# Performance work log

Measured on AMD Instinct MI355X. Metric: run time of the kernel, lower is better.

## Reference

```python
import jax, jax.numpy as jnp
from jax import lax
import numpy as np

B, L, H, V = 256, 2048, 128, 32000
THR = 0.4      # energy_threshold
LN_EPS = 1e-5  # torch LayerNorm default


def setup_inputs() -> dict:
    key = jax.random.key(0)
    ks = jax.random.split(key, 12)
    s = lambda k, shp, scale: (jax.random.normal(k, shp, dtype=jnp.float32) * scale)
    return {
        "seq": jax.random.randint(ks[0], (B, L), 0, V),
        "embed": s(ks[1], (V, H), 0.02),
        "W1": s(ks[2], (H, 2 * H), H ** -0.5),
        "b1": jnp.zeros((2 * H,), jnp.float32),
        "W2": s(ks[3], (2 * H, H), (2 * H) ** -0.5),
        "b2": jnp.zeros((H,), jnp.float32),
        "gamma": jnp.ones((H,), jnp.float32),
        "beta": jnp.zeros((H,), jnp.float32),
        "Wrp": s(ks[4], (H, H), H ** -0.5),
        "brp": jnp.zeros((H,), jnp.float32),
        "Wout": s(ks[5], (H, V), H ** -0.5),
        "bout": jnp.zeros((V,), jnp.float32),
    }


def _encode(seq, embed, W1, b1, W2, b2, gamma, beta):
    e = embed[seq]                                         # [B,L,H]
    ff = jnp.maximum(e @ W1 + b1, 0.0) @ W2 + b2           # [B,L,H]
    y = e + ff
    mu = y.mean(-1, keepdims=True)
    var = ((y - mu) ** 2).mean(-1, keepdims=True)
    return (y - mu) * lax.rsqrt(var + LN_EPS) * gamma + beta


def reference(seq, embed, W1, b1, W2, b2, gamma, beta, Wrp, brp, Wout, bout):
    h_all = _encode(seq, embed, W1, b1, W2, b2, gamma, beta)  # [B,L,H]

    def step(M, k):
        # k = v = h_all[:, t, :]  -> [B,H]
        v = k
        vp = jnp.einsum('bij,bj->bi', M, k)
        error = v - vp / (jnp.sum(k * k, axis=-1, keepdims=True) + 1e-6)
        gate = (jnp.linalg.norm(error, axis=-1)
                > THR * jnp.linalg.norm(v, axis=-1)).astype(M.dtype)  # [B]
        M = M + gate[:, None, None] * jnp.einsum('bi,bj->bij', error, k)
        return M, None

    M0 = jnp.zeros((B, H, H), h_all.dtype)
    ks = jnp.swapaxes(h_all[:, :-1, :], 0, 1)               # [L-1,B,H]
    M_fin, _ = lax.scan(step, M0, ks)
    r = jnp.einsum('bij,bj->bi', M_fin, h_all[:, -1, :])    # [B,H]
    return (r @ Wrp + brp) @ Wout + bout                    # [B,V]
```

## Files before the change

kernel.cpp:

```cpp
#include <hip/hip_runtime.h>
#include <hip/hip_bf16.h>


#define BB 256
#define LL 2048
#define HH 128
#define VV 32000
#define RS 136

typedef float f32x2 __attribute__((ext_vector_type(2)));

__device__ __forceinline__ void dma16(const float* g, float* l) {
  __builtin_amdgcn_global_load_lds(
      (const __attribute__((address_space(1))) void*)g,
      (__attribute__((address_space(3))) void*)l,
      16, 0, 0);
}

template <int CTRL>
__device__ __forceinline__ float dppadd(float x) {
  int y = __builtin_amdgcn_update_dpp(0, __float_as_int(x), CTRL, 0xF, 0xF, true);
  return x + __int_as_float(y);
}

__device__ __forceinline__ void pkfma(f32x2& d, f32x2 a, f32x2 b) {
  asm("v_pk_fma_f32 %0, %1, %2, %0" : "+v"(d) : "v"(a), "v"(b));
}

__device__ __forceinline__ void barrier_lgkm() {
  asm volatile("s_waitcnt lgkmcnt(0)\n\ts_barrier" ::: "memory");
}
__device__ __forceinline__ void wait_vmN(int n) {
  if (n == 5)      asm volatile("s_waitcnt vmcnt(5)" ::: "memory");
  else if (n == 4) asm volatile("s_waitcnt vmcnt(4)" ::: "memory");
  else if (n == 3) asm volatile("s_waitcnt vmcnt(3)" ::: "memory");
  else if (n == 2) asm volatile("s_waitcnt vmcnt(2)" ::: "memory");
  else if (n == 1) asm volatile("s_waitcnt vmcnt(1)" ::: "memory");
  else             asm volatile("s_waitcnt vmcnt(0)" ::: "memory");
}

__global__ __launch_bounds__(256, 1) void build_htab_kernel(
    const float* __restrict__ embed,
    const float* __restrict__ W1,
    const float* __restrict__ b1,
    const float* __restrict__ W2,
    const float* __restrict__ b2,
    const float* __restrict__ gamma,
    const float* __restrict__ beta,
    float* __restrict__ Htab2)
{
  const int tid = threadIdx.x;
  const int j   = tid & 127;
  const int h2  = tid >> 7;

  float w1r[128];
#pragma unroll
  for (int m = 0; m < 128; ++m) w1r[m] = W1[m * 256 + tid];

  const float b1n = b1[tid];
  const float b2j = b2[j];
  const float gj  = gamma[j];
  const float bj  = beta[j];

  __shared__ __align__(16) float4 w2q[64][128];
  __shared__ __align__(16) float e_s[128];
  __shared__ __align__(16) float a_s[256];
  __shared__ float p_s[2][128];
  __shared__ float red[8];

  for (int idx = tid; idx < 8192; idx += 256) {
    int n4 = idx >> 7, jj = idx & 127;
    float4 w;
    w.x = W2[(size_t)(4 * n4 + 0) * 128 + jj];
    w.y = W2[(size_t)(4 * n4 + 1) * 128 + jj];
    w.z = W2[(size_t)(4 * n4 + 2) * 128 + jj];
    w.w = W2[(size_t)(4 * n4 + 3) * 128 + jj];
    w2q[n4][jj] = w;
  }
  __syncthreads();

  for (int v = blockIdx.x; v < VV; v += gridDim.x) {
    if (tid < 128) e_s[tid] = embed[(size_t)v * 128 + tid];
    __syncthreads();

    float acc[4] = {b1n, 0.f, 0.f, 0.f};
#pragma unroll
    for (int q = 0; q < 32; ++q) {
      float4 ev = *(const float4*)&e_s[4 * q];
      float t = ev.x * w1r[4 * q + 0];
      t = fmaf(ev.y, w1r[4 * q + 1], t);
      t = fmaf(ev.z, w1r[4 * q + 2], t);
      t = fmaf(ev.w, w1r[4 * q + 3], t);
      acc[q & 3] += t;
    }
    float a = fmaxf((acc[0] + acc[1]) + (acc[2] + acc[3]), 0.0f);
    a_s[tid] = a;
    __syncthreads();

    float p0 = 0.f, p1 = 0.f, p2v = 0.f, p3 = 0.f;
#pragma unroll
    for (int q = 0; q < 32; ++q) {
      int n4 = h2 * 32 + q;
      float4 av = *(const float4*)&a_s[4 * n4];
      float4 wq = w2q[n4][j];
      p0 = fmaf(av.x, wq.x, p0);
      p1 = fmaf(av.y, wq.y, p1);
      p2v = fmaf(av.z, wq.z, p2v);
      p3 = fmaf(av.w, wq.w, p3);
    }
    p_s[h2][j] = (p0 + p1) + (p2v + p3);
    __syncthreads();

    float y = 0.0f;
    if (tid < 128) {
      float ff = p_s[0][tid] + p_s[1][tid] + b2j;
      y = e_s[tid] + ff;
    }
    float s1 = y, s2 = y * y;
    s1 = dppadd<0xB1>(s1);  s2 = dppadd<0xB1>(s2);
    s1 = dppadd<0x4E>(s1);  s2 = dppadd<0x4E>(s2);
    s1 = dppadd<0x141>(s1); s2 = dppadd<0x141>(s2);
    s1 = dppadd<0x140>(s1); s2 = dppadd<0x140>(s2);
    s1 = dppadd<0x142>(s1); s2 = dppadd<0x142>(s2);
    s1 = dppadd<0x143>(s1); s2 = dppadd<0x143>(s2);
    if (tid < 128 && (tid & 63) == 63) {
      red[tid >> 6] = s1;
      red[2 + (tid >> 6)] = s2;
    }
    __syncthreads();
    float mu = (red[0] + red[1]) * (1.0f / 128.0f);
    float ms = (red[2] + red[3]) * (1.0f / 128.0f);
    float var = ms - mu * mu;
    float hv = 0.0f;
    if (tid < 128) {
      float dy = y - mu;
      hv = dy * (1.0f / sqrtf(var + 1e-5f)) * gj + bj;
      int ofs = tid + ((tid >> 6) << 2);
      Htab2[(size_t)v * RS + ofs] = hv;
    }
    float q2 = hv * hv;
    q2 = dppadd<0xB1>(q2);
    q2 = dppadd<0x4E>(q2);
    q2 = dppadd<0x141>(q2);
    q2 = dppadd<0x140>(q2);
    q2 = dppadd<0x142>(q2);
    q2 = dppadd<0x143>(q2);
    if (tid < 128 && (tid & 63) == 63) red[4 + (tid >> 6)] = q2;
    __syncthreads();
    if (tid == 0) {
      float kk = red[4] + red[5];
      Htab2[(size_t)v * RS + 132] = kk;
      Htab2[(size_t)v * RS + 133] = 1.0f / (kk + 1e-6f);
    }
    __syncthreads();
  }
}

__global__ __launch_bounds__(512, 1) void scan_kernel(
    const int* __restrict__ seq,
    const float* __restrict__ Htab2,
    const float* __restrict__ Wrp,
    const float* __restrict__ brp,
    float* __restrict__ rr)
{
  const int b     = blockIdx.x;
  const int tid   = threadIdx.x;
  const int i     = tid >> 2;
  const int q     = tid & 3;
  const int lane  = tid & 63;
  const int wv    = tid >> 6;
  const int iofs  = i + ((i >> 6) << 2);
  const int kbase = (q & 1) * 32 + (q >> 1) * 68;

  __shared__ int seq_s[LL];
  __shared__ __align__(16) float slots[6][RS];
  __shared__ __align__(16) float2 red2[3][8];
  __shared__ __align__(16) float r_s[128];
  __shared__ float p2_s[4][128];

  {
    for (int jj = 0; jj < 6; ++jj) {
      int tj = seq[(size_t)b * LL + jj];
      if (lane < 34)
        dma16(Htab2 + (size_t)tj * RS + lane * 4, &slots[jj][0]);
    }
  }
  for (int t = tid; t < LL; t += 512) seq_s[t] = seq[(size_t)b * LL + t];
  __syncthreads();

  f32x2 M2[16];
#pragma unroll
  for (int m = 0; m < 16; ++m) M2[m] = f32x2{0.f, 0.f};

  f32x2 kA[16], kB[16], kC[16];
  float kiA, kkA, invA, kiB, kkB, invB;
  float kiC = 0.f, kkC = 0.f, invC = 0.f;
  {
    const float4* kp = (const float4*)&slots[0][kbase];
#pragma unroll
    for (int m = 0; m < 8; ++m) {
      float4 tq = kp[m];
      kA[2 * m]     = f32x2{tq.x, tq.y};
      kA[2 * m + 1] = f32x2{tq.z, tq.w};
    }
    kiA = slots[0][iofs];
    float2 kv = *(const float2*)&slots[0][132];
    kkA = kv.x; invA = kv.y;
  }
  {
    const float4* kp = (const float4*)&slots[1][kbase];
#pragma unroll
    for (int m = 0; m < 8; ++m) {
      float4 tq = kp[m];
      kB[2 * m]     = f32x2{tq.x, tq.y};
      kB[2 * m + 1] = f32x2{tq.z, tq.w};
    }
    kiB = slots[1][iofs];
    float2 kv = *(const float2*)&slots[1][132];
    kkB = kv.x; invB = kv.y;
  }
#pragma unroll
  for (int m = 0; m < 16; ++m) kC[m] = f32x2{0.f, 0.f};

  __syncthreads();

  float e   = kiA;
  float vpb = 0.f;
  int   tk  = seq_s[6];

  auto step = [&](f32x2 (&kc)[16], float ki_c, float kk_c, float inv_c,
                  f32x2 (&kn)[16], float ki_n, float kk_n, float inv_n,
                  f32x2 (&kr)[16], float& ki_r, float& kk_r, float& inv_r,
                  int u, int p, int sn, int sd, int nwait,
                  int do_issue, int do_pref, int do_refill, int do_tail) {
    if (do_issue) {
      if (lane < 34)
        dma16(Htab2 + (size_t)tk * RS + lane * 4, &slots[sd][0]);
    }
    float s  = e * e;
    float c1 = ki_c * ki_n;
    s = dppadd<0x141>(s);  c1 = dppadd<0x141>(c1);
    s = dppadd<0x140>(s);  c1 = dppadd<0x140>(c1);
    s = dppadd<0x142>(s);  c1 = dppadd<0x142>(c1);
    s = dppadd<0x143>(s);  c1 = dppadd<0x143>(c1);
    if (lane == 63) red2[p][wv] = float2{s, c1};
    barrier_lgkm();

    const float4* rp = (const float4*)&red2[p][0];
    float4 ra = rp[0], rb = rp[1], rc = rp[2], rd = rp[3];
    if (do_refill) {
      wait_vmN(nwait);
      const float4* kp = (const float4*)&slots[sn][kbase];
#pragma unroll
      for (int m = 0; m < 8; ++m) {
        float4 tq = kp[m];
        kr[2 * m]     = f32x2{tq.x, tq.y};
        kr[2 * m + 1] = f32x2{tq.z, tq.w};
      }
      ki_r = slots[sn][iofs];
      float2 kv = *(const float2*)&slots[sn][132];
      kk_r = kv.x; inv_r = kv.y;
    }
    if (do_pref) tk = seq_s[u + 7];
    float ne2 = ((ra.x + ra.z) + (rb.x + rb.z)) + ((rc.x + rc.z) + (rd.x + rd.z));
    float cc  = ((ra.y + ra.w) + (rb.y + rb.w)) + ((rc.y + rc.w) + (rd.y + rd.w));
    int  g  = ne2 > 0.16f * kk_c;
    float ge = g ? e : 0.0f;
    float ce = g ? cc : 0.0f;
    float vp = fmaf(ce, e, vpb);
    if (do_tail) { vpb = vp; return; }
    e = fmaf(-vp, inv_n, ki_n);
    f32x2 gev{ge, ge};
#pragma unroll
    for (int m = 0; m < 16; ++m) pkfma(M2[m], gev, kc[m]);
    f32x2 a0{0.f,0.f}, a1{0.f,0.f}, a2{0.f,0.f}, a3{0.f,0.f};
#pragma unroll
    for (int m = 0; m < 4; ++m) {
      pkfma(a0, kr[4 * m + 0], M2[4 * m + 0]);
      pkfma(a1, kr[4 * m + 1], M2[4 * m + 1]);
      pkfma(a2, kr[4 * m + 2], M2[4 * m + 2]);
      pkfma(a3, kr[4 * m + 3], M2[4 * m + 3]);
    }
    float nv = ((a0.x + a0.y) + (a1.x + a1.y)) + ((a2.x + a2.y) + (a3.x + a3.y));
    nv = dppadd<0xB1>(nv);
    nv = dppadd<0x4E>(nv);
    vpb = nv;
  };

  for (int t = 0; t < 2040; t += 6) {
    step(kA, kiA, kkA, invA, kB, kiB, kkB, invB, kC, kiC, kkC, invC,
         t + 0, 0, 2, 0, 4, 1, 1, 1, 0);
    step(kB, kiB, kkB, invB, kC, kiC, kkC, invC, kA, kiA, kkA, invA,
         t + 1, 1, 3, 1, 4, 1, 1, 1, 0);
    step(kC, kiC, kkC, invC, kA, kiA, kkA, invA, kB, kiB, kkB, invB,
         t + 2, 2, 4, 2, 4, 1, 1, 1, 0);
    step(kA, kiA, kkA, invA, kB, kiB, kkB, invB, kC, kiC, kkC, invC,
         t + 3, 0, 5, 3, 4, 1, 1, 1, 0);
    step(kB, kiB, kkB, invB, kC, kiC, kkC, invC, kA, kiA, kkA, invA,
         t + 4, 1, 0, 4, 4, 1, 1, 1, 0);
    step(kC, kiC, kkC, invC, kA, kiA, kkA, invA, kB, kiB, kkB, invB,
         t + 5, 2, 1, 5, 4, 1, 1, 1, 0);
  }
  step(kA, kiA, kkA, invA, kB, kiB, kkB, invB, kC, kiC, kkC, invC,
       2040, 0, 2, 0, 4, 1, 1, 1, 0);
  step(kB, kiB, kkB, invB, kC, kiC, kkC, invC, kA, kiA, kkA, invA,
       2041, 1, 3, 1, 4, 1, 0, 1, 0);
  step(kC, kiC, kkC, invC, kA, kiA, kkA, invA, kB, kiB, kkB, invB,
       2042, 2, 4, 2, 3, 0, 0, 1, 0);
  step(kA, kiA, kkA, invA, kB, kiB, kkB, invB, kC, kiC, kkC, invC,
       2043, 0, 5, 3, 2, 0, 0, 1, 0);
  step(kB, kiB, kkB, invB, kC, kiC, kkC, invC, kA, kiA, kkA, invA,
       2044, 1, 0, 4, 1, 0, 0, 1, 0);
  step(kC, kiC, kkC, invC, kA, kiA, kkA, invA, kB, kiB, kkB, invB,
       2045, 2, 1, 5, 0, 0, 0, 1, 0);
  step(kA, kiA, kkA, invA, kB, kiB, kkB, invB, kC, kiC, kkC, invC,
       2046, 0, 2, 0, 0, 0, 0, 0, 1);

  if (q == 0) r_s[i] = vpb;
  __syncthreads();

  const int j = tid & 127;
  const int g = tid >> 7;
  float pac[2] = {0.f, 0.f};
#pragma unroll
  for (int m = 0; m < 32; ++m) {
    pac[m & 1] = fmaf(r_s[g * 32 + m],
                      Wrp[(size_t)(g * 32 + m) * 128 + j], pac[m & 1]);
  }
  p2_s[g][j] = pac[0] + pac[1];
  __syncthreads();
  if (tid < 128) {
    rr[(size_t)b * 128 + tid] =
        p2_s[0][tid] + p2_s[1][tid] + p2_s[2][tid] + p2_s[3][tid] + brp[tid];
  }
}

__global__ __launch_bounds__(256, 1) void out_kernel(
    const float* __restrict__ rr,
    const float* __restrict__ Wout,
    const float* __restrict__ bout,
    float* __restrict__ out)
{
  const int tid = threadIdx.x;
  const int v = blockIdx.x * 64 + (tid & 63);
  const int bg = tid >> 6;
  const int b0 = blockIdx.y * 64;

  __shared__ float4 rs4[64][32];
  for (int idx = tid; idx < 2048; idx += 256) {
    int bb = idx >> 5, q = idx & 31;
    rs4[bb][q] = ((const float4*)rr)[(size_t)(b0 + bb) * 32 + q];
  }
  __syncthreads();

  float acc[16];
#pragma unroll
  for (int m = 0; m < 16; ++m) acc[m] = 0.0f;

  for (int h4 = 0; h4 < 32; ++h4) {
    float w0 = Wout[(size_t)(4 * h4 + 0) * VV + v];
    float w1 = Wout[(size_t)(4 * h4 + 1) * VV + v];
    float w2 = Wout[(size_t)(4 * h4 + 2) * VV + v];
    float w3 = Wout[(size_t)(4 * h4 + 3) * VV + v];
#pragma unroll
    for (int m = 0; m < 16; ++m) {
      float4 rv = rs4[bg * 16 + m][h4];
      float t = rv.x * w0;
      t = fmaf(rv.y, w1, t);
      t = fmaf(rv.z, w2, t);
      t = fmaf(rv.w, w3, t);
      acc[m] += t;
    }
  }
  float bo = bout[v];
#pragma unroll
  for (int m = 0; m < 16; ++m) {
    out[(size_t)(b0 + bg * 16 + m) * VV + v] = acc[m] + bo;
  }
}

extern "C" void kernel_launch(void* const* d_in, const int* in_sizes, int n_in,
                              void* d_out, int out_size, void* d_ws, size_t ws_size,
                              hipStream_t stream)
{
  const int* seq      = (const int*)d_in[0];
  const float* embed  = (const float*)d_in[1];
  const float* W1     = (const float*)d_in[2];
  const float* b1     = (const float*)d_in[3];
  const float* W2     = (const float*)d_in[4];
  const float* b2     = (const float*)d_in[5];
  const float* gamma  = (const float*)d_in[6];
  const float* beta   = (const float*)d_in[7];
  const float* Wrp    = (const float*)d_in[8];
  const float* brp    = (const float*)d_in[9];
  const float* Wout   = (const float*)d_in[10];
  const float* bout   = (const float*)d_in[11];
  float* out          = (float*)d_out;

  char* ws = (char*)d_ws;
  float* Htab2 = (float*)ws;
  float* rr    = (float*)(ws + 17408000);

  hipLaunchKernelGGL(build_htab_kernel, dim3(256), dim3(256), 0, stream,
                     embed, W1, b1, W2, b2, gamma, beta, Htab2);
  hipLaunchKernelGGL(scan_kernel, dim3(BB), dim3(512), 0, stream,
                     seq, Htab2, Wrp, brp, rr);
  hipLaunchKernelGGL(out_kernel, dim3(VV / 64, 4), dim3(256), 0, stream,
                     rr, Wout, bout, out);
}
```

Before: 1.608 ms.

## Defer rank-1 M update past the barrier and algebraically correct the next prediction

The scan step is reorganised so the gated rank-1 update of M from the previous step is applied after the reduction barrier, and the next matvec uses the not-yet-updated M. The missing contribution is added back through a scalar correction term (ac * e_prev, using the k·k' cross product). This moves the 16 packed FMAs of the update off the serial critical path between barriers, letting them overlap with the barrier wait and the LDS reads. The cost is an extra tail step, a sched_barrier constraint, and slightly different floating-point rounding from the reassociated correction.

Result: slower. 1.679 ms (+4.4%).

```diff
diff --git a/kernel.cpp b/kernel.cpp
--- a/kernel.cpp
+++ b/kernel.cpp
@@ -31,8 +31,7 @@
   asm volatile("s_waitcnt lgkmcnt(0)\n\ts_barrier" ::: "memory");
 }
 __device__ __forceinline__ void wait_vmN(int n) {
-  if (n == 5)      asm volatile("s_waitcnt vmcnt(5)" ::: "memory");
-  else if (n == 4) asm volatile("s_waitcnt vmcnt(4)" ::: "memory");
+  if (n == 4)      asm volatile("s_waitcnt vmcnt(4)" ::: "memory");
   else if (n == 3) asm volatile("s_waitcnt vmcnt(3)" ::: "memory");
   else if (n == 2) asm volatile("s_waitcnt vmcnt(2)" ::: "memory");
   else if (n == 1) asm volatile("s_waitcnt vmcnt(1)" ::: "memory");
@@ -178,12 +177,10 @@
   __shared__ __align__(16) float r_s[128];
   __shared__ float p2_s[4][128];
 
-  {
-    for (int jj = 0; jj < 6; ++jj) {
-      int tj = seq[(size_t)b * LL + jj];
-      if (lane < 34)
-        dma16(Htab2 + (size_t)tj * RS + lane * 4, &slots[jj][0]);
-    }
+  for (int jj = 0; jj < 6; ++jj) {
+    int tj = seq[(size_t)b * LL + jj];
+    if (lane < 34)
+      dma16(Htab2 + (size_t)tj * RS + lane * 4, &slots[jj][0]);
   }
   for (int t = tid; t < LL; t += 512) seq_s[t] = seq[(size_t)b * LL + t];
   __syncthreads();
@@ -193,130 +190,152 @@
   for (int m = 0; m < 16; ++m) M2[m] = f32x2{0.f, 0.f};
 
   f32x2 kA[16], kB[16], kC[16];
-  float kiA, kkA, invA, kiB, kkB, invB;
-  float kiC = 0.f, kkC = 0.f, invC = 0.f;
+  float kiA = 0.f, kkA = 0.f, invA = 0.f;
+  float kiB, kkB, invB, kiC, kkC, invC;
+#pragma unroll
+  for (int m = 0; m < 16; ++m) kA[m] = f32x2{0.f, 0.f};
   {
     const float4* kp = (const float4*)&slots[0][kbase];
-#pragma unroll
-    for (int m = 0; m < 8; ++m) {
-      float4 tq = kp[m];
-      kA[2 * m]     = f32x2{tq.x, tq.y};
-      kA[2 * m + 1] = f32x2{tq.z, tq.w};
-    }
-    kiA = slots[0][iofs];
-    float2 kv = *(const float2*)&slots[0][132];
-    kkA = kv.x; invA = kv.y;
-  }
-  {
-    const float4* kp = (const float4*)&slots[1][kbase];
 #pragma unroll
     for (int m = 0; m < 8; ++m) {
       float4 tq = kp[m];
       kB[2 * m]     = f32x2{tq.x, tq.y};
       kB[2 * m + 1] = f32x2{tq.z, tq.w};
     }
-    kiB = slots[1][iofs];
+    kiB = slots[0][iofs];
+    float2 kv = *(const float2*)&slots[0][132];
+    kkB = kv.x; invB = kv.y;
+  }
+  {
+    const float4* kp = (const float4*)&slots[1][kbase];
+#pragma unroll
+    for (int m = 0; m < 8; ++m) {
+      float4 tq = kp[m];
+      kC[2 * m]     = f32x2{tq.x, tq.y};
+      kC[2 * m + 1] = f32x2{tq.z, tq.w};
+    }
+    kiC = slots[1][iofs];
     float2 kv = *(const float2*)&slots[1][132];
-    kkB = kv.x; invB = kv.y;
-  }
-#pragma unroll
-  for (int m = 0; m < 16; ++m) kC[m] = f32x2{0.f, 0.f};
-
-  __syncthreads();
-
-  float e   = kiA;
-  float vpb = 0.f;
-  int   tk  = seq_s[6];
-
-  auto step = [&](f32x2 (&kc)[16], float ki_c, float kk_c, float inv_c,
-                  f32x2 (&kn)[16], float ki_n, float kk_n, float inv_n,
-                  f32x2 (&kr)[16], float& ki_r, float& kk_r, float& inv_r,
-                  int u, int p, int sn, int sd, int nwait,
-                  int do_issue, int do_pref, int do_refill, int do_tail) {
+    kkC = kv.x; invC = kv.y;
+  }
+  __syncthreads();
+
+  float e_prev  = 0.f;
+  float ge_prev = 0.f;
+  float ac      = 0.f;
+  float vpb     = 0.f;
+  int   tk      = seq_s[6];
+
+  auto step = [&](f32x2 (&kO)[16], float& kiO, float& kkO, float& invO,
+                  f32x2 (&kCc)[16], float& kiCc, float& kkCc, float& invCc,
+                  f32x2 (&kN)[16], float& kiN, float& kkN, float& invN,
+                  int t, int p, int sread, int sdma, int nwait,
+                  int do_issue, int do_pref, int do_refill) {
     if (do_issue) {
       if (lane < 34)
-        dma16(Htab2 + (size_t)tk * RS + lane * 4, &slots[sd][0]);
-    }
+        dma16(Htab2 + (size_t)tk * RS + lane * 4, &slots[sdma][0]);
+    }
+    float e = fmaf(-ac, e_prev, fmaf(-invCc, vpb, kiCc));
     float s  = e * e;
-    float c1 = ki_c * ki_n;
+    float c1 = kiCc * kiN;
     s = dppadd<0x141>(s);  c1 = dppadd<0x141>(c1);
     s = dppadd<0x140>(s);  c1 = dppadd<0x140>(c1);
     s = dppadd<0x142>(s);  c1 = dppadd<0x142>(c1);
     s = dppadd<0x143>(s);  c1 = dppadd<0x143>(c1);
     if (lane == 63) red2[p][wv] = float2{s, c1};
     barrier_lgkm();
-
+    __builtin_amdgcn_sched_barrier(0);
+    {
+      f32x2 gev{ge_prev, ge_prev};
+#pragma unroll
+      for (int m = 0; m < 16; ++m) pkfma(M2[m], gev, kO[m]);
+    }
     const float4* rp = (const float4*)&red2[p][0];
-    float4 ra = rp[0], rb = rp[1], rc = rp[2], rd = rp[3];
-    if (do_refill) {
-      wait_vmN(nwait);
-      const float4* kp = (const float4*)&slots[sn][kbase];
-#pragma unroll
-      for (int m = 0; m < 8; ++m) {
-        float4 tq = kp[m];
-        kr[2 * m]     = f32x2{tq.x, tq.y};
-        kr[2 * m + 1] = f32x2{tq.z, tq.w};
-      }
-      ki_r = slots[sn][iofs];
-      float2 kv = *(const float2*)&slots[sn][132];
-      kk_r = kv.x; inv_r = kv.y;
-    }
-    if (do_pref) tk = seq_s[u + 7];
-    float ne2 = ((ra.x + ra.z) + (rb.x + rb.z)) + ((rc.x + rc.z) + (rd.x + rd.z));
-    float cc  = ((ra.y + ra.w) + (rb.y + rb.w)) + ((rc.y + rc.w) + (rd.y + rd.w));
-    int  g  = ne2 > 0.16f * kk_c;
-    float ge = g ? e : 0.0f;
-    float ce = g ? cc : 0.0f;
-    float vp = fmaf(ce, e, vpb);
-    if (do_tail) { vpb = vp; return; }
-    e = fmaf(-vp, inv_n, ki_n);
-    f32x2 gev{ge, ge};
-#pragma unroll
-    for (int m = 0; m < 16; ++m) pkfma(M2[m], gev, kc[m]);
+    float4 ra = rp[0], rb = rp[1], rc4 = rp[2], rd = rp[3];
     f32x2 a0{0.f,0.f}, a1{0.f,0.f}, a2{0.f,0.f}, a3{0.f,0.f};
 #pragma unroll
     for (int m = 0; m < 4; ++m) {
-      pkfma(a0, kr[4 * m + 0], M2[4 * m + 0]);
-      pkfma(a1, kr[4 * m + 1], M2[4 * m + 1]);
-      pkfma(a2, kr[4 * m + 2], M2[4 * m + 2]);
-      pkfma(a3, kr[4 * m + 3], M2[4 * m + 3]);
+      pkfma(a0, kN[4 * m + 0], M2[4 * m + 0]);
+      pkfma(a1, kN[4 * m + 1], M2[4 * m + 1]);
+      pkfma(a2, kN[4 * m + 2], M2[4 * m + 2]);
+      pkfma(a3, kN[4 * m + 3], M2[4 * m + 3]);
     }
     float nv = ((a0.x + a0.y) + (a1.x + a1.y)) + ((a2.x + a2.y) + (a3.x + a3.y));
     nv = dppadd<0xB1>(nv);
     nv = dppadd<0x4E>(nv);
-    vpb = nv;
+    if (do_refill) {
+      wait_vmN(nwait);
+      const float4* kp = (const float4*)&slots[sread][kbase];
+#pragma unroll
+      for (int m = 0; m < 8; ++m) {
+        float4 tq = kp[m];
+        kO[2 * m]     = f32x2{tq.x, tq.y};
+        kO[2 * m + 1] = f32x2{tq.z, tq.w};
+      }
+      kiO = slots[sread][iofs];
+      float2 kv = *(const float2*)&slots[sread][132];
+      kkO = kv.x; invO = kv.y;
+    }
+    if (do_pref) tk = seq_s[t + 7];
+    float ne2 = ((ra.x + ra.z) + (rb.x + rb.z)) + ((rc4.x + rc4.z) + (rd.x + rd.z));
+    float cs  = ((ra.y + ra.w) + (rb.y + rb.w)) + ((rc4.y + rc4.w) + (rd.y + rd.w));
+    int  g  = ne2 > 0.16f * kkCc;
+    ge_prev = g ? e : 0.0f;
+    ac      = g ? (invN * cs) : 0.0f;
+    e_prev  = e;
+    vpb     = nv;
   };
 
   for (int t = 0; t < 2040; t += 6) {
-    step(kA, kiA, kkA, invA, kB, kiB, kkB, invB, kC, kiC, kkC, invC,
-         t + 0, 0, 2, 0, 4, 1, 1, 1, 0);
-    step(kB, kiB, kkB, invB, kC, kiC, kkC, invC, kA, kiA, kkA, invA,
-         t + 1, 1, 3, 1, 4, 1, 1, 1, 0);
-    step(kC, kiC, kkC, invC, kA, kiA, kkA, invA, kB, kiB, kkB, invB,
-         t + 2, 2, 4, 2, 4, 1, 1, 1, 0);
-    step(kA, kiA, kkA, invA, kB, kiB, kkB, invB, kC, kiC, kkC, invC,
-         t + 3, 0, 5, 3, 4, 1, 1, 1, 0);
-    step(kB, kiB, kkB, invB, kC, kiC, kkC, invC, kA, kiA, kkA, invA,
-         t + 4, 1, 0, 4, 4, 1, 1, 1, 0);
-    step(kC, kiC, kkC, invC, kA, kiA, kkA, invA, kB, kiB, kkB, invB,
-         t + 5, 2, 1, 5, 4, 1, 1, 1, 0);
-  }
-  step(kA, kiA, kkA, invA, kB, kiB, kkB, invB, kC, kiC, kkC, invC,
-       2040, 0, 2, 0, 4, 1, 1, 1, 0);
-  step(kB, kiB, kkB, invB, kC, kiC, kkC, invC, kA, kiA, kkA, invA,
-       2041, 1, 3, 1, 4, 1, 0, 1, 0);
-  step(kC, kiC, kkC, invC, kA, kiA, kkA, invA, kB, kiB, kkB, invB,
-       2042, 2, 4, 2, 3, 0, 0, 1, 0);
-  step(kA, kiA, kkA, invA, kB, kiB, kkB, invB, kC, kiC, kkC, invC,
-       2043, 0, 5, 3, 2, 0, 0, 1, 0);
-  step(kB, kiB, kkB, invB, kC, kiC, kkC, invC, kA, kiA, kkA, invA,
-       2044, 1, 0, 4, 1, 0, 0, 1, 0);
-  step(kC, kiC, kkC, invC, kA, kiA, kkA, invA, kB, kiB, kkB, invB,
-       2045, 2, 1, 5, 0, 0, 0, 1, 0);
-  step(kA, kiA, kkA, invA, kB, kiB, kkB, invB, kC, kiC, kkC, invC,
-       2046, 0, 2, 0, 0, 0, 0, 0, 1);
-
-  if (q == 0) r_s[i] = vpb;
+    step(kA,kiA,kkA,invA, kB,kiB,kkB,invB, kC,kiC,kkC,invC, t+0, 0, 2, 0, 4, 1,1,1);
+    step(kB,kiB,kkB,invB, kC,kiC,kkC,invC, kA,kiA,kkA,invA, t+1, 1, 3, 1, 4, 1,1,1);
+    step(kC,kiC,kkC,invC, kA,kiA,kkA,invA, kB,kiB,kkB,invB, t+2, 2, 4, 2, 4, 1,1,1);
+    step(kA,kiA,kkA,invA, kB,kiB,kkB,invB, kC,kiC,kkC,invC, t+3, 0, 5, 3, 4, 1,1,1);
+    step(kB,kiB,kkB,invB, kC,kiC,kkC,invC, kA,kiA,kkA,invA, t+4, 1, 0, 4, 4, 1,1,1);
+    step(kC,kiC,kkC,invC, kA,kiA,kkA,invA, kB,kiB,kkB,invB, t+5, 2, 1, 5, 4, 1,1,1);
+  }
+  step(kA,kiA,kkA,invA, kB,kiB,kkB,invB, kC,kiC,kkC,invC, 2040, 0, 2, 0, 4, 1,1,1);
+  step(kB,kiB,kkB,invB, kC,kiC,kkC,invC, kA,kiA,kkA,invA, 2041, 1, 3, 1, 4, 1,0,1);
+  step(kC,kiC,kkC,invC, kA,kiA,kkA,invA, kB,kiB,kkB,invB, 2042, 2, 4, 2, 3, 0,0,1);
+  step(kA,kiA,kkA,invA, kB,kiB,kkB,invB, kC,kiC,kkC,invC, 2043, 0, 5, 3, 2, 0,0,1);
+  step(kB,kiB,kkB,invB, kC,kiC,kkC,invC, kA,kiA,kkA,invA, 2044, 1, 0, 4, 1, 0,0,1);
+  step(kC,kiC,kkC,invC, kA,kiA,kkA,invA, kB,kiB,kkB,invB, 2045, 2, 1, 5, 0, 0,0,1);
+  {
+    float e = fmaf(-ac, e_prev, fmaf(-invB, vpb, kiB));
+    float s  = e * e;
+    float c1 = kiB * kiC;
+    s = dppadd<0x141>(s);  c1 = dppadd<0x141>(c1);
+    s = dppadd<0x140>(s);  c1 = dppadd<0x140>(c1);
+    s = dppadd<0x142>(s);  c1 = dppadd<0x142>(c1);
+    s = dppadd<0x143>(s);  c1 = dppadd<0x143>(c1);
+    if (lane == 63) red2[0][wv] = float2{s, c1};
+    barrier_lgkm();
+    __builtin_amdgcn_sched_barrier(0);
+    {
+      f32x2 gev{ge_prev, ge_prev};
+#pragma unroll
+      for (int m = 0; m < 16; ++m) pkfma(M2[m], gev, kA[m]);
+    }
+    const float4* rp = (const float4*)&red2[0][0];
+    float4 ra = rp[0], rb = rp[1], rc4 = rp[2], rd = rp[3];
+    f32x2 a0{0.f,0.f}, a1{0.f,0.f}, a2{0.f,0.f}, a3{0.f,0.f};
+#pragma unroll
+    for (int m = 0; m < 4; ++m) {
+      pkfma(a0, kC[4 * m + 0], M2[4 * m + 0]);
+      pkfma(a1, kC[4 * m + 1], M2[4 * m + 1]);
+      pkfma(a2, kC[4 * m + 2], M2[4 * m + 2]);
+      pkfma(a3, kC[4 * m + 3], M2[4 * m + 3]);
+    }
+    float nv = ((a0.x + a0.y) + (a1.x + a1.y)) + ((a2.x + a2.y) + (a3.x + a3.y));
+    nv = dppadd<0xB1>(nv);
+    nv = dppadd<0x4E>(nv);
+    float ne2 = ((ra.x + ra.z) + (rb.x + rb.z)) + ((rc4.x + rc4.z) + (rd.x + rd.z));
+    float cs  = ((ra.y + ra.w) + (rb.y + rb.w)) + ((rc4.y + rc4.w) + (rd.y + rd.w));
+    int  g  = ne2 > 0.16f * kkB;
+    float gc = g ? cs : 0.0f;
+    float rres = fmaf(gc, e, nv);
+    if (q == 0) r_s[i] = rres;
+  }
   __syncthreads();
 
   const int j = tid & 127;
```
